# Kernel tuning notes

Hardware: AMD Instinct MI355X
Metric: run time of the kernel (lower is better)

## Reference

```python
import jax, jax.numpy as jnp
import numpy as np
from jax import lax

SEQ, B, I, H, OUT = 256, 64, 256, 1024, 1024


def setup_inputs() -> dict:
    key = jax.random.key(0)
    ks = jax.random.split(key, 9)
    s_i = 1.0 / np.sqrt(I)
    s_h = 1.0 / np.sqrt(H)
    s_f = 1.0 / np.sqrt(2 * H)
    # Gate order: i, f, o, c (stacked along last dim -> 4H). Biases of the
    # x-linear and h-linear are summed in the cell, so a single combined bias
    # per gate is mathematically identical.
    return {
        "x": jax.random.normal(ks[0], (SEQ, B, I), dtype=jnp.float32),
        "Wx_f": jax.random.uniform(ks[1], (I, 4 * H), jnp.float32, -s_i, s_i),
        "Wh_f": jax.random.uniform(ks[2], (H, 4 * H), jnp.float32, -s_h, s_h),
        "b_f": jax.random.uniform(ks[3], (4 * H,), jnp.float32, -s_h, s_h),
        "Wx_b": jax.random.uniform(ks[4], (I, 4 * H), jnp.float32, -s_i, s_i),
        "Wh_b": jax.random.uniform(ks[5], (H, 4 * H), jnp.float32, -s_h, s_h),
        "b_b": jax.random.uniform(ks[6], (4 * H,), jnp.float32, -s_h, s_h),
        "W_fc": jax.random.uniform(ks[7], (2 * H, OUT), jnp.float32, -s_f, s_f),
        "b_fc": jax.random.uniform(ks[8], (OUT,), jnp.float32, -s_f, s_f),
    }


def _lstm_dir(x, Wx, Wh, b, reverse):
    B_, H_ = x.shape[1], Wh.shape[0]
    # Precompute input projections for all timesteps in one big GEMM.
    xg = jnp.einsum("tbi,ig->tbg", x, Wx) + b  # [T, B, 4H]

    def step(carry, xg_t):
        c, h = carry
        g = xg_t + h @ Wh  # [B, 4H]
        i, f, o, cg = jnp.split(g, 4, axis=-1)
        new_c = jax.nn.sigmoid(f) * c + jax.nn.sigmoid(i) * jnp.tanh(cg)
        new_h = jax.nn.sigmoid(o) * jnp.tanh(new_c)
        return (new_c, new_h), new_h

    init = (jnp.zeros((B_, H_), x.dtype), jnp.zeros((B_, H_), x.dtype))
    (c_last, h_last), hs = lax.scan(step, init, xg, reverse=reverse)
    # lax.scan(reverse=True) returns hs aligned to the original time order,
    # matching outputs_backward.insert(0, ...) in the torch code.
    return hs, h_last, c_last


def reference(x, Wx_f, Wh_f, b_f, Wx_b, Wh_b, b_b, W_fc, b_fc):
    hs_f, hF, cF = _lstm_dir(x, Wx_f, Wh_f, b_f, reverse=False)
    hs_b, hB, cB = _lstm_dir(x, Wx_b, Wh_b, b_b, reverse=True)
    combined = jnp.concatenate([hs_f, hs_b], axis=-1)  # [T, B, 2H]
    outputs = jnp.einsum("tbh,ho->tbo", combined, W_fc) + b_fc
    return outputs, ((hF, hB), (cF, cB))
```

## Files before the change

### kernel.cpp

```cpp
#include <hip/hip_runtime.h>

using short8 = __attribute__((ext_vector_type(8))) short;
using f32x4  = __attribute__((ext_vector_type(4))) float;

typedef unsigned short u16;
typedef unsigned int   u32;
typedef unsigned long long u64;

#define T_SEQ 256
#define BATCH 64
#define INP   256
#define HID   1024
#define GDIM  4096
#define KC    1280
#define OUTD  1024

#define NSL   40
#define NBLK  256
#define DBLK  128
#define LDSB  (NSL * 2 * 64 * 8 * 2)

#define MFMA16(a,b,c) __builtin_amdgcn_mfma_f32_16x16x32_bf16(a,b,c,0,0,0)

__device__ __forceinline__ u16 f2bf(float f){
  union { float f; u32 u; } v; v.f = f;
  u32 r = v.u + 0x7fffu + ((v.u >> 16) & 1u);
  return (u16)(r >> 16);
}
__device__ __forceinline__ float sigm(float x){ return 1.f/(1.f+__expf(-x)); }
__device__ __forceinline__ float tanhf_(float x){ return 1.f - 2.f/(__expf(2.f*x)+1.f); }

__device__ __forceinline__ void ag_st_u32(u32* p, u32 v){
  __hip_atomic_store(p, v, __ATOMIC_RELAXED, __HIP_MEMORY_SCOPE_AGENT);
}
__device__ __forceinline__ u64 ag_ld_u64(const u64* p){
  return __hip_atomic_load(p, __ATOMIC_RELAXED, __HIP_MEMORY_SCOPE_AGENT);
}

template<int CTRL>
__device__ __forceinline__ float qperm(float v){
  union { float f; int i; } u; u.f = v;
  u.i = __builtin_amdgcn_mov_dpp(u.i, CTRL, 0xf, 0xf, true);
  return u.f;
}
#define QP_XOR1 177
#define QP_XOR2 78

__global__ void build_wc(const float* __restrict__ WhF, const float* __restrict__ WxF,
                         const float* __restrict__ WhB, const float* __restrict__ WxB,
                         u16* __restrict__ WcF, u16* __restrict__ WcB)
{
  const int z = blockIdx.z; const int dir = z >> 2, gate = z & 3;
  const float* Wh = dir ? WhB : WhF;
  const float* Wx = dir ? WxB : WxF;
  u16* Wc = dir ? WcB : WcF;
  const int k0 = blockIdx.x * 64, j0 = blockIdx.y * 64;
  __shared__ float tile[64][65];
  const int t = threadIdx.x;
  #pragma unroll
  for (int i = 0; i < 16; ++i) {
    int idx = i*256 + t; int kr = idx >> 6, jc = idx & 63;
    int k = k0 + kr;
    float v = (k < HID) ? Wh[(size_t)k*GDIM + gate*HID + j0 + jc]
                        : Wx[(size_t)(k-HID)*GDIM + gate*HID + j0 + jc];
    tile[kr][jc] = v;
  }
  __syncthreads();
  #pragma unroll
  for (int i = 0; i < 16; ++i) {
    int idx = i*256 + t; int jc = idx >> 6, kr = idx & 63;
    int j  = j0 + jc;
    int nb = j >> 3, jl = j & 7;
    int nt = jl & 1, rq = jl >> 1;
    int n  = nb*32 + nt*16 + rq*4 + gate;
    Wc[(size_t)n*KC + k0 + kr] = f2bf(tile[kr][jc]);
  }
}

__global__ void build_wfc(const float* __restrict__ Wfc, u16* __restrict__ WfcT)
{
  const int k0 = blockIdx.x * 64;
  const int n0 = blockIdx.y * 64;
  __shared__ float tile[64][65];
  const int t = threadIdx.x;
  #pragma unroll
  for (int i = 0; i < 16; ++i) {
    int idx = i*256 + t; int kr = idx >> 6, nc = idx & 63;
    tile[kr][nc] = Wfc[(size_t)(k0+kr)*OUTD + n0 + nc];
  }
  __syncthreads();
  #pragma unroll
  for (int i = 0; i < 16; ++i) {
    int idx = i*256 + t; int nc = idx >> 6, kr = idx & 63;
    WfcT[(size_t)(n0+nc)*2048 + k0 + kr] = f2bf(tile[kr][nc]);
  }
}

__global__ void conv_x(const float* __restrict__ x, u16* __restrict__ xb, int n)
{
  int i = (blockIdx.x * blockDim.x + threadIdx.x) * 4;
  if (i < n) {
    float4 v = *(const float4*)(x + i);
    u32 lo = (u32)f2bf(v.x) | ((u32)f2bf(v.y) << 16);
    u32 hi = (u32)f2bf(v.z) | ((u32)f2bf(v.w) << 16);
    *(uint2*)(xb + i) = make_uint2(lo, hi);
  }
}

__global__ __launch_bounds__(256, 1) void lstm_persist(
    const u16* __restrict__ WcF, const u16* __restrict__ WcB,
    const u16* __restrict__ xb,
    const float* __restrict__ bF, const float* __restrict__ bB,
    u16* __restrict__ hs, float* __restrict__ out_tail, int* flags)
{
  extern __shared__ __align__(16) u16 Bs[];

  __builtin_amdgcn_fence(__ATOMIC_ACQUIRE, "agent");

  const int bid = blockIdx.x;
  const int dir = bid >> 7;
  const int nb  = bid & 127;
  const int n0  = nb * 32;
  const u16* __restrict__ Wc   = dir ? WcB : WcF;
  const float* __restrict__ bias = dir ? bB : bF;

  const int tid  = threadIdx.x;
  const int w    = tid >> 6, lane = tid & 63;
  const int r    = lane & 15, q = lane >> 4, rq = r >> 2;
  int* __restrict__ fl = flags + (dir * 4 + w) * DBLK;
  const u64* __restrict__ fl64 = (const u64*)fl;

  for (int c = tid; c < NSL * 128; c += 256) {
    int ks  = c >> 7;
    int rem = c & 127;
    int nt  = rem >> 6, l2 = rem & 63;
    *(short8*)&Bs[(size_t)c * 8] =
        *(const short8*)(Wc + (size_t)(n0 + nt*16 + (l2 & 15)) * KC + ks*32 + (l2 >> 4)*8);
  }
  #define BSF(ks, nt) (*(const short8*)&Bs[((size_t)(((ks)*2 + (nt))*64 + lane))*8])

  const int jbase = nb * 8;
  float bia[2][4];
  #pragma unroll
  for (int nt = 0; nt < 2; ++nt)
    #pragma unroll
    for (int g = 0; g < 4; ++g)
      bia[nt][g] = bias[g * HID + jbase + 2*rq + nt];

  float creg[2][4];
  #pragma unroll
  for (int nt = 0; nt < 2; ++nt)
    #pragma unroll
    for (int rg = 0; rg < 4; ++rg) creg[nt][rg] = 0.f;

  const int row_a = w * 16 + r;

  short8 xf[8];
  {
    const int tt0 = dir ? (T_SEQ - 1) : 0;
    const u16* axr = xb + ((size_t)tt0 * BATCH + row_a) * INP;
    #pragma unroll
    for (int kx = 0; kx < 8; ++kx) xf[kx] = *(const short8*)(axr + kx*32 + q*8);
  }
  __syncthreads();

  f32x4 accA[2], accB[2];
  accA[0] = (f32x4)(0.f); accA[1] = (f32x4)(0.f);
  accB[0] = (f32x4)(0.f); accB[1] = (f32x4)(0.f);
  #pragma unroll
  for (int kx = 0; kx < 8; ++kx) {
    accA[0] = MFMA16(xf[kx], BSF(32 + kx, 0), accA[0]);
    accA[1] = MFMA16(xf[kx], BSF(32 + kx, 1), accA[1]);
  }

  u64 pf = 0;

  for (int s = 0; s < T_SEQ; ++s) {
    const int tt = dir ? (T_SEQ - 1 - s) : s;

    if (s > 0) {
      while (true) {
        int ok = ((int)(pf & 0xffffffffu) >= s) && ((int)(pf >> 32) >= s);
        if (__all(ok)) break;
        __builtin_amdgcn_s_sleep(1);
        pf = ag_ld_u64(fl64 + lane);
      }
      const int tp = dir ? tt + 1 : tt - 1;
      const u16* __restrict__ ar =
          hs + ((size_t)tp * BATCH + row_a) * 2048 + dir * HID;
      short8 hA[32];
      #pragma unroll
      for (int i = 0; i < 32; ++i) hA[i] = *(const short8*)(ar + i*32 + q*8);
      __builtin_amdgcn_sched_group_barrier(0x20, 32, 0);
      #pragma unroll
      for (int i = 0; i < 16; ++i) {
        accA[0] = MFMA16(hA[i], BSF(i, 0), accA[0]);
        accA[1] = MFMA16(hA[i], BSF(i, 1), accA[1]);
        accB[0] = MFMA16(hA[16 + i], BSF(16 + i, 0), accB[0]);
        accB[1] = MFMA16(hA[16 + i], BSF(16 + i, 1), accB[1]);
      }
      __builtin_amdgcn_sched_group_barrier(0x8, 64, 0);
    }

    float hnv[2][4];
    #pragma unroll
    for (int nt = 0; nt < 2; ++nt) {
      #pragma unroll
      for (int rg = 0; rg < 4; ++rg) {
        float v  = accA[nt][rg] + accB[nt][rg];
        float x1 = qperm<QP_XOR1>(v);
        float x2 = qperm<QP_XOR2>(v);
        float x3 = qperm<QP_XOR2>(x1);
        float cn = sigm(x1 + bia[nt][1]) * creg[nt][rg] + sigm(v + bia[nt][0]) * tanhf_(x3 + bia[nt][3]);
        float hn = sigm(x2 + bia[nt][2]) * tanhf_(cn);
        creg[nt][rg] = cn; hnv[nt][rg] = hn;
      }
    }
    if ((r & 3) == 0) {
      #pragma unroll
      for (int rg = 0; rg < 4; ++rg) {
        int row = w * 16 + q * 4 + rg;
        u32 packed = (u32)f2bf(hnv[0][rg]) | ((u32)f2bf(hnv[1][rg]) << 16);
        ag_st_u32((u32*)(hs + ((size_t)tt * BATCH + row) * 2048 + dir * HID + jbase + 2*rq),
                  packed);
      }
    }

    if (s < T_SEQ - 1) {
      asm volatile("s_waitcnt vmcnt(0)" ::: "memory");
      if (lane == 0) ag_st_u32((u32*)(fl + nb), (u32)(s + 1));
      const int tn = dir ? tt - 1 : tt + 1;
      const u16* axr = xb + ((size_t)tn * BATCH + row_a) * INP;
      #pragma unroll
      for (int kx = 0; kx < 8; ++kx) xf[kx] = *(const short8*)(axr + kx*32 + q*8);
      pf = ag_ld_u64(fl64 + lane);
      accA[0] = (f32x4)(0.f); accA[1] = (f32x4)(0.f);
      accB[0] = (f32x4)(0.f); accB[1] = (f32x4)(0.f);
      #pragma unroll
      for (int kx = 0; kx < 8; ++kx) {
        accA[0] = MFMA16(xf[kx], BSF(32 + kx, 0), accA[0]);
        accA[1] = MFMA16(xf[kx], BSF(32 + kx, 1), accA[1]);
      }
    } else {
      if ((r & 3) == 0) {
        #pragma unroll
        for (int nt = 0; nt < 2; ++nt)
          #pragma unroll
          for (int rg = 0; rg < 4; ++rg) {
            int row = w * 16 + q * 4 + rg;
            int j   = jbase + 2*rq + nt;
            out_tail[dir * (BATCH * HID) + (size_t)row * HID + j] = hnv[nt][rg];
            out_tail[2 * (BATCH * HID) + dir * (BATCH * HID) + (size_t)row * HID + j] = creg[nt][rg];
          }
      }
    }
  }
  #undef BSF
}

__global__ __launch_bounds__(256) void fc_kernel(
    const u16* __restrict__ hs, const u16* __restrict__ WfcT,
    const float* __restrict__ bfc, float* __restrict__ out)
{
  const int m0 = blockIdx.x * 128, n0 = blockIdx.y * 128;
  __shared__ __align__(16) u16 As[128 * 32];
  __shared__ __align__(16) u16 Bs[128 * 32];
  const int tid = threadIdx.x;
  const int w = tid >> 6, lane = tid & 63;
  const int r = lane & 15, q = lane >> 4;
  const int wy = w >> 1, wx = w & 1;

  f32x4 acc[4][4];
  #pragma unroll
  for (int a = 0; a < 4; ++a)
    #pragma unroll
    for (int b = 0; b < 4; ++b) acc[a][b] = (f32x4)(0.f);

  const int lr = tid >> 1, lk = (tid & 1) * 16;

  for (int k0 = 0; k0 < 2048; k0 += 32) {
    __syncthreads();
    *(short8*)&As[lr * 32 + lk]     = *(const short8*)(hs   + (size_t)(m0 + lr) * 2048 + k0 + lk);
    *(short8*)&As[lr * 32 + lk + 8] = *(const short8*)(hs   + (size_t)(m0 + lr) * 2048 + k0 + lk + 8);
    *(short8*)&Bs[lr * 32 + lk]     = *(const short8*)(WfcT + (size_t)(n0 + lr) * 2048 + k0 + lk);
    *(short8*)&Bs[lr * 32 + lk + 8] = *(const short8*)(WfcT + (size_t)(n0 + lr) * 2048 + k0 + lk + 8);
    __syncthreads();

    short8 af[4], bf[4];
    #pragma unroll
    for (int mt = 0; mt < 4; ++mt)
      af[mt] = *(const short8*)&As[(wy * 64 + mt * 16 + r) * 32 + q * 8];
    #pragma unroll
    for (int nt = 0; nt < 4; ++nt)
      bf[nt] = *(const short8*)&Bs[(wx * 64 + nt * 16 + r) * 32 + q * 8];
    #pragma unroll
    for (int mt = 0; mt < 4; ++mt)
      #pragma unroll
      for (int nt = 0; nt < 4; ++nt)
        acc[mt][nt] = __builtin_amdgcn_mfma_f32_16x16x32_bf16(af[mt], bf[nt], acc[mt][nt], 0, 0, 0);
  }

  #pragma unroll
  for (int mt = 0; mt < 4; ++mt)
    #pragma unroll
    for (int nt = 0; nt < 4; ++nt)
      #pragma unroll
      for (int reg = 0; reg < 4; ++reg) {
        int m = m0 + wy * 64 + mt * 16 + q * 4 + reg;
        int n = n0 + wx * 64 + nt * 16 + r;
        out[(size_t)m * OUTD + n] = acc[mt][nt][reg] + bfc[n];
      }
}

extern "C" void kernel_launch(void* const* d_in, const int* in_sizes, int n_in,
                              void* d_out, int out_size, void* d_ws, size_t ws_size,
                              hipStream_t stream)
{
  const float* x   = (const float*)d_in[0];
  const float* WxF = (const float*)d_in[1];
  const float* WhF = (const float*)d_in[2];
  const float* bF  = (const float*)d_in[3];
  const float* WxB = (const float*)d_in[4];
  const float* WhB = (const float*)d_in[5];
  const float* bB  = (const float*)d_in[6];
  const float* Wfc = (const float*)d_in[7];
  const float* bfc = (const float*)d_in[8];
  float* out = (float*)d_out;

  char* ws = (char*)d_ws;
  u16*  WcF   = (u16*)(ws + 0);
  u16*  WcB   = (u16*)(ws + 10485760);
  u16*  WfcT  = (u16*)(ws + 20971520);
  u16*  xb    = (u16*)(ws + 25165824);
  u16*  hs    = (u16*)(ws + 34603008);
  int*  flags = (int*)(ws + 101711872);

  hipMemsetAsync(flags, 0, 4096, stream);

  hipFuncSetAttribute((const void*)lstm_persist,
                      hipFuncAttributeMaxDynamicSharedMemorySize, LDSB);

  build_wc <<<dim3(KC/64, HID/64, 8), 256, 0, stream>>>(WhF, WxF, WhB, WxB, WcF, WcB);
  build_wfc<<<dim3(2048/64, OUTD/64), 256, 0, stream>>>(Wfc, WfcT);
  conv_x   <<<(T_SEQ*BATCH*INP)/4/256, 256, 0, stream>>>(x, xb, T_SEQ*BATCH*INP);

  lstm_persist<<<NBLK, 256, LDSB, stream>>>(WcF, WcB, xb, bF, bB,
                                            hs, out + 16777216, flags);

  fc_kernel<<<dim3(16384/128, OUTD/128), 256, 0, stream>>>(hs, WfcT, bfc, out);
}
```

Before: 2.943 ms.

## Tile hidden-state buffer so per-step h reads and writes are coalesced

Replaces the row-major [t][b][2H] bf16 hidden-state buffer with a blocked layout grouped by (time, direction, 8-column block, batch row). Each block's h writes then land contiguously, and the recurrent A-operand loads become 16-byte reads with a fixed stride. This is meant to cut memory transactions on the serial critical path. The FC kernel's A loads are rewritten to the new layout, the spin-wait sleep is removed, and the scheduling group barriers are dropped, which changes the instruction schedule and raises polling traffic.

```diff
diff --git a/kernel.cpp b/kernel.cpp
--- a/kernel.cpp
+++ b/kernel.cpp
@@ -111,7 +111,7 @@
     const u16* __restrict__ WcF, const u16* __restrict__ WcB,
     const u16* __restrict__ xb,
     const float* __restrict__ bF, const float* __restrict__ bB,
-    u16* __restrict__ hs, float* __restrict__ out_tail, int* flags)
+    u32* __restrict__ hs2, float* __restrict__ out_tail, int* flags)
 {
   extern __shared__ __align__(16) u16 Bs[];
 
@@ -182,16 +182,15 @@
       while (true) {
         int ok = ((int)(pf & 0xffffffffu) >= s) && ((int)(pf >> 32) >= s);
         if (__all(ok)) break;
-        __builtin_amdgcn_s_sleep(1);
         pf = ag_ld_u64(fl64 + lane);
       }
       const int tp = dir ? tt + 1 : tt - 1;
-      const u16* __restrict__ ar =
-          hs + ((size_t)tp * BATCH + row_a) * 2048 + dir * HID;
+      const u32* __restrict__ ar =
+          hs2 + (((size_t)(tp * 2 + dir) * 128 + q) * 64 + row_a) * 4;
       short8 hA[32];
       #pragma unroll
-      for (int i = 0; i < 32; ++i) hA[i] = *(const short8*)(ar + i*32 + q*8);
-      __builtin_amdgcn_sched_group_barrier(0x20, 32, 0);
+      for (int i = 0; i < 32; ++i)
+        hA[i] = *(const short8*)(ar + (size_t)i * 1024);
       #pragma unroll
       for (int i = 0; i < 16; ++i) {
         accA[0] = MFMA16(hA[i], BSF(i, 0), accA[0]);
@@ -199,7 +198,6 @@
         accB[0] = MFMA16(hA[16 + i], BSF(16 + i, 0), accB[0]);
         accB[1] = MFMA16(hA[16 + i], BSF(16 + i, 1), accB[1]);
       }
-      __builtin_amdgcn_sched_group_barrier(0x8, 64, 0);
     }
 
     float hnv[2][4];
@@ -217,12 +215,11 @@
       }
     }
     if ((r & 3) == 0) {
+      u32* base = hs2 + (((size_t)(tt * 2 + dir) * 128 + nb) * 64 + w*16 + q*4) * 4 + rq;
       #pragma unroll
       for (int rg = 0; rg < 4; ++rg) {
-        int row = w * 16 + q * 4 + rg;
         u32 packed = (u32)f2bf(hnv[0][rg]) | ((u32)f2bf(hnv[1][rg]) << 16);
-        ag_st_u32((u32*)(hs + ((size_t)tt * BATCH + row) * 2048 + dir * HID + jbase + 2*rq),
-                  packed);
+        ag_st_u32(base + rg * 4, packed);
       }
     }
 
@@ -259,7 +256,7 @@
 }
 
 __global__ __launch_bounds__(256) void fc_kernel(
-    const u16* __restrict__ hs, const u16* __restrict__ WfcT,
+    const u32* __restrict__ hs2, const u16* __restrict__ WfcT,
     const float* __restrict__ bfc, float* __restrict__ out)
 {
   const int m0 = blockIdx.x * 128, n0 = blockIdx.y * 128;
@@ -280,8 +277,13 @@
 
   for (int k0 = 0; k0 < 2048; k0 += 32) {
     __syncthreads();
-    *(short8*)&As[lr * 32 + lk]     = *(const short8*)(hs   + (size_t)(m0 + lr) * 2048 + k0 + lk);
-    *(short8*)&As[lr * 32 + lk + 8] = *(const short8*)(hs   + (size_t)(m0 + lr) * 2048 + k0 + lk + 8);
+    {
+      int m = m0 + lr; int t = m >> 6, row = m & 63;
+      int k = k0 + lk; int d = k >> 10, kk = k & 1023; int nb2 = kk >> 3;
+      const u32* p = hs2 + (((size_t)(t * 2 + d) * 128 + nb2) * 64 + row) * 4;
+      *(short8*)&As[lr * 32 + lk]     = *(const short8*)p;
+      *(short8*)&As[lr * 32 + lk + 8] = *(const short8*)(p + 256);
+    }
     *(short8*)&Bs[lr * 32 + lk]     = *(const short8*)(WfcT + (size_t)(n0 + lr) * 2048 + k0 + lk);
     *(short8*)&Bs[lr * 32 + lk + 8] = *(const short8*)(WfcT + (size_t)(n0 + lr) * 2048 + k0 + lk + 8);
     __syncthreads();
@@ -332,7 +334,7 @@
   u16*  WcB   = (u16*)(ws + 10485760);
   u16*  WfcT  = (u16*)(ws + 20971520);
   u16*  xb    = (u16*)(ws + 25165824);
-  u16*  hs    = (u16*)(ws + 34603008);
+  u32*  hs2   = (u32*)(ws + 34603008);
   int*  flags = (int*)(ws + 101711872);
 
   hipMemsetAsync(flags, 0, 4096, stream);
@@ -345,7 +347,7 @@
   conv_x   <<<(T_SEQ*BATCH*INP)/4/256, 256, 0, stream>>>(x, xb, T_SEQ*BATCH*INP);
 
   lstm_persist<<<NBLK, 256, LDSB, stream>>>(WcF, WcB, xb, bF, bB,
-                                            hs, out + 16777216, flags);
-
-  fc_kernel<<<dim3(16384/128, OUTD/128), 256, 0, stream>>>(hs, WfcT, bfc, out);
-}
+                                            hs2, out + 16777216, flags);
+
+  fc_kernel<<<dim3(16384/128, OUTD/128), 256, 0, stream>>>(hs2, WfcT, bfc, out);
+}
```

Result: faster. 2.410 ms (-18.1%).
